# Performance work log

Hardware: AMD Instinct MI355X
Metric: run time of the kernel (lower is better)

## Reference

```python
import jax, jax.numpy as jnp
import numpy as np

NUM_CLS = 80
NUM_CONVS = 4
GROUPS = 32
STRIDES = [8, 16, 32, 64, 128]
SIZES = [32.0, 64.0, 128.0, 256.0, 512.0]
CLS_BIAS_INIT = -float(np.log((1 - 0.01) / 0.01))


def _conv(x, w, b):
    # NCHW 3x3 stride-1 same-pad conv
    y = jax.lax.conv_general_dilated(x, w, (1, 1), 'SAME',
                                     dimension_numbers=('NCHW', 'OIHW', 'NCHW'))
    return y + b[None, :, None, None]


def _group_norm(x, gamma, beta, eps=1e-5):
    B, C, H, W = x.shape
    xr = x.reshape(B, GROUPS, C // GROUPS, H, W)
    m = xr.mean(axis=(2, 3, 4), keepdims=True)
    v = xr.var(axis=(2, 3, 4), keepdims=True)
    xn = ((xr - m) / jnp.sqrt(v + eps)).reshape(B, C, H, W)
    return xn * gamma[None, :, None, None] + beta[None, :, None, None]


def _tower(x, ws, bs, gs, betas):
    # CGR block: Conv -> GroupNorm -> ReLU, repeated NUM_CONVS times
    for i in range(NUM_CONVS):
        x = jax.nn.relu(_group_norm(_conv(x, ws[i], bs[i]), gs[i], betas[i]))
    return x


def _build_anchors(h, w, stride, size):
    half = size / 2.0  # single scale=1, ratio=1 -> one square anchor per cell
    yv, xv = jnp.meshgrid(jnp.arange(h, dtype=jnp.float32),
                          jnp.arange(w, dtype=jnp.float32), indexing='ij')
    grid = jnp.stack([xv, yv, xv, yv], axis=-1)  # [h,w,4]
    delta = jnp.array([-half, -half, half, half], dtype=jnp.float32)
    return ((grid + 0.5) * stride + delta).reshape(-1, 4)  # [h*w,4]


def setup_inputs() -> dict:
    key = jax.random.key(0)
    ks = jax.random.split(key, 16)
    C = 256
    feats = {}
    hw = [80, 40, 20, 10, 5]
    for i, name in enumerate(['p3', 'p4', 'p5', 'p6', 'p7']):
        feats[name] = jax.random.normal(ks[i], (8, C, hw[i], hw[i]), dtype=jnp.float32)
    std = 0.01
    inp = dict(feats)
    # cls tower
    inp['cls_tw'] = jax.random.normal(ks[5], (NUM_CONVS, C, C, 3, 3), jnp.float32) * std
    inp['cls_tb'] = jnp.zeros((NUM_CONVS, C), jnp.float32)
    inp['cls_tg'] = jnp.ones((NUM_CONVS, C), jnp.float32)
    inp['cls_tbeta'] = jnp.zeros((NUM_CONVS, C), jnp.float32)
    # reg tower
    inp['reg_tw'] = jax.random.normal(ks[6], (NUM_CONVS, C, C, 3, 3), jnp.float32) * std
    inp['reg_tb'] = jnp.zeros((NUM_CONVS, C), jnp.float32)
    inp['reg_tg'] = jnp.ones((NUM_CONVS, C), jnp.float32)
    inp['reg_tbeta'] = jnp.zeros((NUM_CONVS, C), jnp.float32)
    # heads (num_anchors = 1)
    inp['cls_hw'] = jax.random.normal(ks[7], (NUM_CLS, C, 3, 3), jnp.float32) * std
    inp['cls_hb'] = jnp.full((NUM_CLS,), CLS_BIAS_INIT, jnp.float32)
    inp['reg_hw'] = jax.random.normal(ks[8], (4, C, 3, 3), jnp.float32) * std
    inp['reg_hb'] = jnp.zeros((4,), jnp.float32)
    inp['iou_hw'] = jax.random.normal(ks[9], (1, C, 3, 3), jnp.float32) * std
    inp['iou_hb'] = jnp.zeros((1,), jnp.float32)
    inp['scales'] = jnp.ones((5,), jnp.float32)
    return inp


def reference(p3, p4, p5, p6, p7,
              cls_tw, cls_tb, cls_tg, cls_tbeta,
              reg_tw, reg_tb, reg_tg, reg_tbeta,
              cls_hw, cls_hb, reg_hw, reg_hb, iou_hw, iou_hb, scales):
    feats = [p3, p4, p5, p6, p7]
    outs = []
    for j, x in enumerate(feats):
        B, _, H, W = x.shape
        ct = _tower(x, cls_tw, cls_tb, cls_tg, cls_tbeta)
        rt = _tower(x, reg_tw, reg_tb, reg_tg, reg_tbeta)
        # heads: permute to NHWC then flatten spatial (num_anchors=1)
        cls = _conv(ct, cls_hw, cls_hb).transpose(0, 2, 3, 1).reshape(B, -1, NUM_CLS)
        reg = _conv(rt, reg_hw, reg_hb).transpose(0, 2, 3, 1).reshape(B, -1, 4) * scales[j]
        iou = _conv(rt, iou_hw, iou_hb).transpose(0, 2, 3, 1).reshape(B, -1, 1)  # on_reg=True
        # decode boxes against anchors
        anchor = _build_anchors(H, W, STRIDES[j], SIZES[j])  # [HW,4]
        awh = anchor[:, 2:] - anchor[:, :2]
        actr = anchor[:, :2] + 0.5 * awh
        xy = reg[..., :2] * awh + actr
        wh = jnp.exp(reg[..., 2:]) * awh
        box = jnp.concatenate([xy - 0.5 * wh, xy + 0.5 * wh], axis=-1)
        outs.append(jnp.concatenate([box, iou, cls], axis=-1))
    return jnp.concatenate(outs, axis=1)  # [B, 8525, 85]
```

## Files before the change

### kernel.cpp

```cpp
#include <hip/hip_runtime.h>
#include <stdint.h>

typedef unsigned short u16;
typedef unsigned int u32;
typedef short short8 __attribute__((ext_vector_type(8)));
typedef float f32x4 __attribute__((ext_vector_type(4)));

struct LevelTab {
  int Hf[5], Wf[5], Hp[5], Wp[5], HW[5], M[5], mtcum[5], aoff[5];
  long xoffp[5], moff[5], ppcum[5], mcum[5];
  float asize[5], astride[5];
};

__device__ __forceinline__ u16 f2bf(float f) {
  u32 u = __float_as_uint(f);
  u = (u + 0x7fffu + ((u >> 16) & 1u)) >> 16;
  return (u16)u;
}
__device__ __forceinline__ float bflo(u32 v) { return __uint_as_float(v << 16); }
__device__ __forceinline__ float bfhi(u32 v) { return __uint_as_float(v & 0xffff0000u); }

__device__ __forceinline__ void gload16(const void* g, void* l) {
  __builtin_amdgcn_global_load_lds((__attribute__((address_space(1))) void*)(g),
                                   (__attribute__((address_space(3))) void*)(l),
                                   16, 0, 0);
}

__global__ __launch_bounds__(256) void prep_tower_w(const float* __restrict__ cls_tw,
                                                    const float* __restrict__ reg_tw,
                                                    u16* __restrict__ W2t) {
  long t = (long)blockIdx.x * 256 + threadIdx.x;
  const long total = 2L * 4 * 256 * 2304;
  if (t >= total) return;
  int ci = (int)(t & 255);
  long u = t >> 8;
  int j = (int)(u % 9); u /= 9;
  int co = (int)(u & 255); u >>= 8;
  int layer = (int)(u & 3);
  int tw = (int)(u >> 2);
  const float* src = tw ? reg_tw : cls_tw;
  float v = src[(((long)layer * 256 + co) * 256 + ci) * 9 + j];
  W2t[t] = f2bf(v);
}

__global__ __launch_bounds__(256) void prep_cls_w(const float* __restrict__ cls_hw,
                                                  u16* __restrict__ W2c) {
  long t = (long)blockIdx.x * 256 + threadIdx.x;
  if (t >= 128L * 2304) return;
  int ci = (int)(t & 255);
  long u = t >> 8;
  int j = (int)(u % 9);
  int co = (int)(u / 9);
  float v = (co < 80) ? cls_hw[(((long)co * 256 + ci) * 9 + j)] : 0.f;
  W2c[t] = f2bf(v);
}

__global__ __launch_bounds__(256) void prep_reg_w(const float* __restrict__ reg_hw,
                                                  const float* __restrict__ iou_hw,
                                                  u16* __restrict__ W2r) {
  long t = (long)blockIdx.x * 256 + threadIdx.x;
  if (t >= 5L * 2304) return;
  int ci = (int)(t & 255);
  long u = t >> 8;
  int j = (int)(u % 9);
  int o = (int)(u / 9);
  float v = (o < 4) ? reg_hw[(((long)o * 256 + ci) * 9 + j)] : iou_hw[(long)ci * 9 + j];
  W2r[t] = f2bf(v);
}

__global__ __launch_bounds__(256) void convert_in(const float* __restrict__ i0, const float* __restrict__ i1,
                                                  const float* __restrict__ i2, const float* __restrict__ i3,
                                                  const float* __restrict__ i4, u16* __restrict__ X0,
                                                  LevelTab lt) {
  long t = (long)blockIdx.x * 256 + threadIdx.x;
  if (t >= lt.ppcum[4] * 32) return;
  const int c8 = (int)(t & 31);
  long pp = t >> 5;
  int lvl = 0;
#pragma unroll
  for (int i = 0; i < 4; ++i) lvl += (pp >= lt.ppcum[i]);
  const long lp = pp - (lvl ? lt.ppcum[lvl - 1] : 0);
  const int Hp = lt.Hp[lvl], Wp = lt.Wp[lvl], Wf = lt.Wf[lvl], HW = lt.HW[lvl];
  const int HpWp = Hp * Wp;
  const int n = (int)(lp / HpWp);
  const int rem = (int)(lp - (long)n * HpWp);
  const int yp = rem / Wp, xp = rem - yp * Wp;
  u16* op = X0 + (lt.xoffp[lvl] + lp) * 256 + c8 * 8;
  if (yp == 0 || yp == Hp - 1 || xp == 0 || xp == Wp - 1) {
    *(uint4*)op = make_uint4(0u, 0u, 0u, 0u);
    return;
  }
  const float* src = lvl == 0 ? i0 : lvl == 1 ? i1 : lvl == 2 ? i2 : lvl == 3 ? i3 : i4;
  const int y = yp - 1, x = xp - 1;
  const long sb = ((long)n * 256 + c8 * 8) * HW + (long)y * Wf + x;
  u32 o4[4];
#pragma unroll
  for (int i = 0; i < 4; ++i) {
    float f0 = src[sb + (long)(2 * i) * HW];
    float f1 = src[sb + (long)(2 * i + 1) * HW];
    o4[i] = (u32)f2bf(f0) | ((u32)f2bf(f1) << 16);
  }
  *(uint4*)op = make_uint4(o4[0], o4[1], o4[2], o4[3]);
}

template <int MODE>
__global__ __launch_bounds__(256, 2) void conv_mfma(
    const u16* __restrict__ XpadA, const u16* __restrict__ XpadB,
    const u16* __restrict__ W2A, const u16* __restrict__ W2B,
    const float* __restrict__ biasA, const float* __restrict__ biasB,
    u16* __restrict__ OtmpA, u16* __restrict__ OtmpB,
    float* __restrict__ Oout, int NP, LevelTab lt) {
  __shared__ __align__(16) u16 sA[3][128 * 32];
  __shared__ __align__(16) u16 sB[3][128 * 32];

  const int nwg = gridDim.x;
  const int qq = nwg >> 3, rr = nwg & 7;
  const int xcd = blockIdx.x & 7, ib = blockIdx.x >> 3;
  const int sid = (xcd < rr ? xcd * (qq + 1) : rr * (qq + 1) + (xcd - rr) * qq) + ib;

  int path, tileId, nt;
  if (MODE == 0) {
    const int tn = (NP == 2) ? (sid >> 1) : sid;
    path = (NP == 2) ? (sid & 1) : 0;
    tileId = tn >> 1;
    nt = tn & 1;
  } else {
    path = 0;
    tileId = sid;
    nt = 0;
  }
  const u16* __restrict__ Xpad = path ? XpadB : XpadA;
  const u16* __restrict__ W2 = path ? W2B : W2A;
  const float* __restrict__ bias = path ? biasB : biasA;
  u16* __restrict__ Otmp = path ? OtmpB : OtmpA;

  int lvl = 0;
#pragma unroll
  for (int i = 0; i < 4; ++i) lvl += (tileId >= lt.mtcum[i]);
  const int mt = tileId - (lvl ? lt.mtcum[lvl - 1] : 0);
  const int Hp = lt.Hp[lvl], Wp = lt.Wp[lvl], Wf = lt.Wf[lvl];
  const int HW = lt.HW[lvl], M = lt.M[lvl];
  const long xbase = lt.xoffp[lvl] * 256;

  const int tid = threadIdx.x;
  const int w = tid >> 6, lane = tid & 63;
  const int rsub = lane >> 2;
  const int r0 = w * 16 + rsub;
  const int q2 = ((lane & 3) - ((lane >> 3) & 3)) & 3;

  long gA[2], gB[2];
#pragma unroll
  for (int i = 0; i < 2; ++i) {
    int ml = mt * 128 + r0 + i * 64;
    if (ml > M - 1) ml = M - 1;
    const int n = ml / HW;
    const int pr = ml - n * HW;
    const int y = pr / Wf;
    const int x = pr - y * Wf;
    gA[i] = xbase + ((long)((n * Hp + y) * Wp + x)) * 256 + q2 * 8;
    gB[i] = (long)(nt * 128 + r0 + i * 64) * 2304 + q2 * 8;
  }

  const int wm = w >> 1, wn = w & 1;
  const int lm = lane & 15;
  const int slot8 = ((((lane >> 4) + ((lane >> 1) & 3)) & 3) << 3);

  f32x4 acc[4][4];
#pragma unroll
  for (int a = 0; a < 4; ++a)
#pragma unroll
    for (int c = 0; c < 4; ++c) acc[a][c] = {0.f, 0.f, 0.f, 0.f};

  auto STAGE = [&](int kk, int buf) {
    const int j = kk >> 3;
    const int c0 = (kk & 7) << 5;
    const int jy = j / 3, jx = j - jy * 3;
    const long aK = ((long)(jy * Wp + jx)) * 256 + c0;
    const long bK = (long)kk << 5;
    gload16(Xpad + gA[0] + aK, sA[buf] + w * 512);
    gload16(Xpad + gA[1] + aK, sA[buf] + 2048 + w * 512);
    gload16(W2 + gB[0] + bK, sB[buf] + w * 512);
    gload16(W2 + gB[1] + bK, sB[buf] + 2048 + w * 512);
  };

  short8 a0[4], b0[4], a1[4], b1[4];
  auto FRAG0 = [&](int cur) {
    const u16* pa = sA[cur];
    const u16* pb = sB[cur];
#pragma unroll
    for (int mi = 0; mi < 4; ++mi)
      a0[mi] = *(const short8*)(pa + ((wm * 64 + mi * 16 + lm) << 5) + slot8);
#pragma unroll
    for (int ni = 0; ni < 4; ++ni)
      b0[ni] = *(const short8*)(pb + ((wn * 64 + ni * 16 + lm) << 5) + slot8);
  };
  auto FRAG1 = [&](int cur) {
    const u16* pa = sA[cur];
    const u16* pb = sB[cur];
#pragma unroll
    for (int mi = 0; mi < 4; ++mi)
      a1[mi] = *(const short8*)(pa + ((wm * 64 + mi * 16 + lm) << 5) + slot8);
#pragma unroll
    for (int ni = 0; ni < 4; ++ni)
      b1[ni] = *(const short8*)(pb + ((wn * 64 + ni * 16 + lm) << 5) + slot8);
  };
  auto MFMA0 = [&]() {
    __builtin_amdgcn_s_setprio(1);
#pragma unroll
    for (int mi = 0; mi < 4; ++mi)
#pragma unroll
      for (int ni = 0; ni < 4; ++ni)
        acc[mi][ni] = __builtin_amdgcn_mfma_f32_16x16x32_bf16(a0[mi], b0[ni], acc[mi][ni], 0, 0, 0);
    __builtin_amdgcn_s_setprio(0);
  };
  auto MFMA1 = [&]() {
    __builtin_amdgcn_s_setprio(1);
#pragma unroll
    for (int mi = 0; mi < 4; ++mi)
#pragma unroll
      for (int ni = 0; ni < 4; ++ni)
        acc[mi][ni] = __builtin_amdgcn_mfma_f32_16x16x32_bf16(a1[mi], b1[ni], acc[mi][ni], 0, 0, 0);
    __builtin_amdgcn_s_setprio(0);
  };

  STAGE(0, 0);
  STAGE(1, 1);
  asm volatile("s_waitcnt vmcnt(4)" ::: "memory");
  __builtin_amdgcn_s_barrier();
  FRAG0(0);
  STAGE(2, 2);

  int rd = 1;
  int st = 0;
  for (int kk = 0; kk < 68; kk += 2) {
    asm volatile("s_waitcnt vmcnt(4)" ::: "memory");
    __builtin_amdgcn_s_barrier();
    FRAG1(rd);
    rd = rd == 2 ? 0 : rd + 1;
    STAGE(kk + 3, st);
    st = st == 2 ? 0 : st + 1;
    MFMA0();
    asm volatile("s_waitcnt vmcnt(4)" ::: "memory");
    __builtin_amdgcn_s_barrier();
    FRAG0(rd);
    rd = rd == 2 ? 0 : rd + 1;
    STAGE(kk + 4, st);
    st = st == 2 ? 0 : st + 1;
    MFMA1();
  }
  asm volatile("s_waitcnt vmcnt(4)" ::: "memory");
  __builtin_amdgcn_s_barrier();
  FRAG1(rd);
  rd = rd == 2 ? 0 : rd + 1;
  STAGE(71, st);
  MFMA0();
  asm volatile("s_waitcnt vmcnt(4)" ::: "memory");
  __builtin_amdgcn_s_barrier();
  FRAG0(rd);
  rd = rd == 2 ? 0 : rd + 1;
  MFMA1();
  asm volatile("s_waitcnt vmcnt(0)" ::: "memory");
  __builtin_amdgcn_s_barrier();
  FRAG1(rd);
  MFMA0();
  MFMA1();

  const int mwb = mt * 128 + wm * 64;
  const int colb = nt * 128 + wn * 64;
  const int rq4 = (lane >> 4) << 2;
#pragma unroll
  for (int ni = 0; ni < 4; ++ni) {
    const int col = colb + ni * 16 + lm;
    if (MODE == 1 && col >= 80) continue;
    const float bv = bias[col];
#pragma unroll
    for (int mi = 0; mi < 4; ++mi) {
      const int rb = mwb + mi * 16 + rq4;
#pragma unroll
      for (int rg = 0; rg < 4; ++rg) {
        const int ml = rb + rg;
        if (ml < M) {
          const float v = acc[mi][ni][rg] + bv;
          if (MODE == 0) {
            Otmp[(lt.moff[lvl] + ml) * 256 + col] = f2bf(v);
          } else {
            const int nb = ml / HW;
            const int pr = ml - nb * HW;
            Oout[((long)nb * 8525 + lt.aoff[lvl] + pr) * 85 + 5 + col] = v;
          }
        }
      }
    }
  }
}

__global__ __launch_bounds__(256) void gn_stats(const u16* __restrict__ tmpA,
                                                const u16* __restrict__ tmpB,
                                                float* __restrict__ stats, LevelTab lt) {
  const int bid = blockIdx.x;
  const int path = bid / 1280;
  const int lb = bid - path * 1280;
  const u16* __restrict__ tmp = path ? tmpB : tmpA;
  const int lvl = lb >> 8, bg = lb & 255, b = bg >> 5, g = bg & 31;
  const int HW = lt.HW[lvl];
  const long base = (lt.moff[lvl] + (long)b * HW) * 256 + g * 8;
  float s = 0.f, ss = 0.f;
  for (int p = threadIdx.x; p < HW; p += 256) {
    const uint4 r = *(const uint4*)(tmp + base + (long)p * 256);
    const u32 u[4] = {r.x, r.y, r.z, r.w};
#pragma unroll
    for (int i = 0; i < 4; ++i) {
      float f0 = bflo(u[i]), f1 = bfhi(u[i]);
      s += f0 + f1;
      ss += f0 * f0 + f1 * f1;
    }
  }
#pragma unroll
  for (int o = 32; o; o >>= 1) {
    s += __shfl_down(s, o);
    ss += __shfl_down(ss, o);
  }
  __shared__ float rs[4], rss[4];
  const int w = threadIdx.x >> 6, lane = threadIdx.x & 63;
  if (lane == 0) { rs[w] = s; rss[w] = ss; }
  __syncthreads();
  if (threadIdx.x == 0) {
    s = rs[0] + rs[1] + rs[2] + rs[3];
    ss = rss[0] + rss[1] + rss[2] + rss[3];
    const float inv = 1.f / (float)(HW * 8);
    const float mean = s * inv;
    const float var = ss * inv - mean * mean;
    stats[bid * 2 + 0] = mean;
    stats[bid * 2 + 1] = rsqrtf(var + 1e-5f);
  }
}

__global__ __launch_bounds__(256) void gn_apply(const u16* __restrict__ tmpA,
                                                const u16* __restrict__ tmpB,
                                                const float* __restrict__ stats,
                                                const float* __restrict__ gammaA,
                                                const float* __restrict__ betaA,
                                                const float* __restrict__ gammaB,
                                                const float* __restrict__ betaB,
                                                u16* __restrict__ poutA, u16* __restrict__ poutB,
                                                int ppBlocks, LevelTab lt) {
  const int path = blockIdx.x / ppBlocks;
  const int xb = blockIdx.x - path * ppBlocks;
  const u16* __restrict__ tmp = path ? tmpB : tmpA;
  const float* __restrict__ gamma = path ? gammaB : gammaA;
  const float* __restrict__ beta = path ? betaB : betaA;
  u16* __restrict__ pout = path ? poutB : poutA;

  long t = (long)xb * 256 + threadIdx.x;
  if (t >= lt.ppcum[4] * 32) return;
  const int c8 = (int)(t & 31);
  long pp = t >> 5;
  int lvl = 0;
#pragma unroll
  for (int i = 0; i < 4; ++i) lvl += (pp >= lt.ppcum[i]);
  const long lp = pp - (lvl ? lt.ppcum[lvl - 1] : 0);
  const int Hp = lt.Hp[lvl], Wp = lt.Wp[lvl], Wf = lt.Wf[lvl], HW = lt.HW[lvl];
  const int HpWp = Hp * Wp;
  const int n = (int)(lp / HpWp);
  const int rem = (int)(lp - (long)n * HpWp);
  const int yp = rem / Wp, xp = rem - yp * Wp;
  u16* op = pout + (lt.xoffp[lvl] + lp) * 256 + c8 * 8;
  if (yp == 0 || yp == Hp - 1 || xp == 0 || xp == Wp - 1) {
    *(uint4*)op = make_uint4(0u, 0u, 0u, 0u);
    return;
  }
  const long m = lt.moff[lvl] + (long)n * HW + (long)(yp - 1) * Wf + (xp - 1);
  const uint4 r = *(const uint4*)(tmp + m * 256 + c8 * 8);
  const int sidx = (path * 1280 + lvl * 256 + n * 32 + c8) * 2;
  const float mean = stats[sidx], rstd = stats[sidx + 1];
  const u32 u[4] = {r.x, r.y, r.z, r.w};
  u32 o4[4];
#pragma unroll
  for (int i = 0; i < 4; ++i) {
    const int c = c8 * 8 + i * 2;
    float f0 = (bflo(u[i]) - mean) * rstd * gamma[c] + beta[c];
    float f1 = (bfhi(u[i]) - mean) * rstd * gamma[c + 1] + beta[c + 1];
    f0 = fmaxf(f0, 0.f);
    f1 = fmaxf(f1, 0.f);
    o4[i] = (u32)f2bf(f0) | ((u32)f2bf(f1) << 16);
  }
  *(uint4*)op = make_uint4(o4[0], o4[1], o4[2], o4[3]);
}

__global__ __launch_bounds__(256) void regiou_decode(const u16* __restrict__ Xp,
                                                     const u16* __restrict__ W2r,
                                                     const float* __restrict__ reg_hb,
                                                     const float* __restrict__ iou_hb,
                                                     const float* __restrict__ scales,
                                                     float* __restrict__ out, LevelTab lt) {
  const long gt = (long)blockIdx.x * 256 + threadIdx.x;
  const int gw = (int)(gt >> 6);
  const int lane = threadIdx.x & 63;
  if (gw >= (int)lt.mcum[4]) return;
  int lvl = 0;
#pragma unroll
  for (int i = 0; i < 4; ++i) lvl += (gw >= (int)lt.mcum[i]);
  const int m = gw - (int)(lvl ? lt.mcum[lvl - 1] : 0);
  const int HW = lt.HW[lvl], Wf = lt.Wf[lvl], Hp = lt.Hp[lvl], Wp = lt.Wp[lvl];
  const int b = m / HW, pr = m - b * HW;
  const int y = pr / Wf, x = pr - y * Wf;
  const long base = (lt.xoffp[lvl] + (long)(b * Hp + y) * Wp + x) * 256 + lane * 4;
  float acc[5] = {0.f, 0.f, 0.f, 0.f, 0.f};
#pragma unroll
  for (int j = 0; j < 9; ++j) {
    const int jy = j / 3, jx = j - jy * 3;
    const uint2 ar = *(const uint2*)(Xp + base + ((long)(jy * Wp + jx)) * 256);
    const float x0 = bflo(ar.x), x1 = bfhi(ar.x), x2 = bflo(ar.y), x3 = bfhi(ar.y);
#pragma unroll
    for (int o = 0; o < 5; ++o) {
      const uint2 wr = *(const uint2*)(W2r + o * 2304 + j * 256 + lane * 4);
      acc[o] += x0 * bflo(wr.x) + x1 * bfhi(wr.x) + x2 * bflo(wr.y) + x3 * bfhi(wr.y);
    }
  }
#pragma unroll
  for (int o = 0; o < 5; ++o)
#pragma unroll
    for (int d = 32; d; d >>= 1) acc[o] += __shfl_down(acc[o], d);
  if (lane == 0) {
    const float sc = scales[lvl];
    const float r0 = (acc[0] + reg_hb[0]) * sc;
    const float r1 = (acc[1] + reg_hb[1]) * sc;
    const float r2 = (acc[2] + reg_hb[2]) * sc;
    const float r3 = (acc[3] + reg_hb[3]) * sc;
    const float iou = acc[4] + iou_hb[0];
    const float st = lt.astride[lvl], sz = lt.asize[lvl];
    const float cx = (x + 0.5f) * st, cy = (y + 0.5f) * st;
    const float xx = r0 * sz + cx, yy = r1 * sz + cy;
    const float ww = expf(r2) * sz, hh = expf(r3) * sz;
    float* o = out + ((long)b * 8525 + lt.aoff[lvl] + pr) * 85;
    o[0] = xx - 0.5f * ww;
    o[1] = yy - 0.5f * hh;
    o[2] = xx + 0.5f * ww;
    o[3] = yy + 0.5f * hh;
    o[4] = iou;
  }
}

extern "C" void kernel_launch(void* const* d_in, const int* in_sizes, int n_in, void* d_out,
                              int out_size, void* d_ws, size_t ws_size, hipStream_t stream) {
  const float* feats[5];
  for (int i = 0; i < 5; ++i) feats[i] = (const float*)d_in[i];
  const float* cls_tw = (const float*)d_in[5];
  const float* cls_tb = (const float*)d_in[6];
  const float* cls_tg = (const float*)d_in[7];
  const float* cls_tbeta = (const float*)d_in[8];
  const float* reg_tw = (const float*)d_in[9];
  const float* reg_tb = (const float*)d_in[10];
  const float* reg_tg = (const float*)d_in[11];
  const float* reg_tbeta = (const float*)d_in[12];
  const float* cls_hw = (const float*)d_in[13];
  const float* cls_hb = (const float*)d_in[14];
  const float* reg_hw = (const float*)d_in[15];
  const float* reg_hb = (const float*)d_in[16];
  const float* iou_hw = (const float*)d_in[17];
  const float* iou_hb = (const float*)d_in[18];
  const float* scales = (const float*)d_in[19];
  float* out = (float*)d_out;

  LevelTab lt;
  const int Hs[5] = {80, 40, 20, 10, 5};
  const float sizes[5] = {32.f, 64.f, 128.f, 256.f, 512.f};
  const float strides[5] = {8.f, 16.f, 32.f, 64.f, 128.f};
  long ppc = 0, mc = 0;
  int mtc = 0, ao = 0;
  for (int i = 0; i < 5; ++i) {
    const int H = Hs[i];
    lt.Hf[i] = H; lt.Wf[i] = H; lt.Hp[i] = H + 2; lt.Wp[i] = H + 2;
    lt.HW[i] = H * H; lt.M[i] = 8 * H * H;
    lt.xoffp[i] = ppc; lt.moff[i] = mc; lt.aoff[i] = ao;
    ppc += 8L * (H + 2) * (H + 2);
    mc += lt.M[i];
    mtc += (lt.M[i] + 127) / 128;
    lt.ppcum[i] = ppc; lt.mcum[i] = mc; lt.mtcum[i] = mtc;
    ao += H * H;
    lt.asize[i] = sizes[i]; lt.astride[i] = strides[i];
  }

  char* ws = (char*)d_ws;
  size_t off = 0;
  auto take = [&](size_t bytes) {
    off = (off + 255) & ~(size_t)255;
    char* p = ws + off;
    off += bytes;
    return p;
  };
  auto alg = [](size_t v) { return (v + 255) & ~(size_t)255; };
  const size_t sizeX = alg((size_t)ppc * 512);
  const size_t sizeT = alg((size_t)mc * 512);
  const size_t wTsz = alg((size_t)2 * 4 * 256 * 2304 * 2);
  const size_t wCsz = alg((size_t)128 * 2304 * 2);
  const size_t wRsz = alg((size_t)5 * 2304 * 2);
  const size_t sSsz = alg((size_t)2 * 1280 * 2 * 4);
  const size_t needMerged = 4 * sizeX + 2 * sizeT + wTsz + wCsz + wRsz + sSsz + 4096;
  const bool MERGED = (ws_size >= needMerged);

  const int ppBlocks = (int)((ppc * 32 + 255) / 256);

  if (MERGED) {
    u16* X0 = (u16*)take(sizeX);
    u16* C1 = (u16*)take(sizeX);
    u16* R0 = (u16*)take(sizeX);
    u16* R1 = (u16*)take(sizeX);
    u16* tmpA = (u16*)take(sizeT);
    u16* tmpB = (u16*)take(sizeT);
    u16* W2t = (u16*)take(wTsz);
    u16* W2c = (u16*)take(wCsz);
    u16* W2r = (u16*)take(wRsz);
    float* stats = (float*)take(sSsz);

    prep_tower_w<<<(int)((2L * 4 * 256 * 2304 + 255) / 256), 256, 0, stream>>>(cls_tw, reg_tw, W2t);
    prep_cls_w<<<(int)((128L * 2304 + 255) / 256), 256, 0, stream>>>(cls_hw, W2c);
    prep_reg_w<<<(int)((5L * 2304 + 255) / 256), 256, 0, stream>>>(reg_hw, iou_hw, W2r);
    convert_in<<<ppBlocks, 256, 0, stream>>>(feats[0], feats[1], feats[2], feats[3], feats[4], X0, lt);

    u16* wrA[4] = {X0, C1, X0, C1};
    u16* wrB[4] = {R0, R1, R0, R1};
    const u16* curA = X0;
    const u16* curB = X0;
    for (int layer = 0; layer < 4; ++layer) {
      const u16* w2A = W2t + (size_t)(0 * 4 + layer) * 256 * 2304;
      const u16* w2B = W2t + (size_t)(1 * 4 + layer) * 256 * 2304;
      conv_mfma<0><<<mtc * 2 * 2, 256, 0, stream>>>(curA, curB, w2A, w2B,
                                                    cls_tb + layer * 256, reg_tb + layer * 256,
                                                    tmpA, tmpB, nullptr, 2, lt);
      gn_stats<<<2 * 1280, 256, 0, stream>>>(tmpA, tmpB, stats, lt);
      gn_apply<<<2 * ppBlocks, 256, 0, stream>>>(tmpA, tmpB, stats,
                                                 cls_tg + layer * 256, cls_tbeta + layer * 256,
                                                 reg_tg + layer * 256, reg_tbeta + layer * 256,
                                                 wrA[layer], wrB[layer], ppBlocks, lt);
      curA = wrA[layer];
      curB = wrB[layer];
    }
    conv_mfma<1><<<mtc, 256, 0, stream>>>(curA, curA, W2c, W2c, cls_hb, cls_hb,
                                          nullptr, nullptr, out, 1, lt);
    regiou_decode<<<(int)((mc * 64 + 255) / 256), 256, 0, stream>>>(curB, W2r, reg_hb, iou_hb,
                                                                    scales, out, lt);
  } else {
    u16* X0 = (u16*)take(sizeX);
    u16* padA = (u16*)take(sizeX);
    u16* padB = (u16*)take(sizeX);
    u16* tmp = (u16*)take(sizeT);
    u16* W2t = (u16*)take(wTsz);
    u16* W2c = (u16*)take(wCsz);
    u16* W2r = (u16*)take(wRsz);
    float* stats = (float*)take(sSsz);

    prep_tower_w<<<(int)((2L * 4 * 256 * 2304 + 255) / 256), 256, 0, stream>>>(cls_tw, reg_tw, W2t);
    prep_cls_w<<<(int)((128L * 2304 + 255) / 256), 256, 0, stream>>>(cls_hw, W2c);
    prep_reg_w<<<(int)((5L * 2304 + 255) / 256), 256, 0, stream>>>(reg_hw, iou_hw, W2r);
    convert_in<<<ppBlocks, 256, 0, stream>>>(feats[0], feats[1], feats[2], feats[3], feats[4], X0, lt);

    u16* pads[2] = {padA, padB};
    for (int tw = 0; tw < 2; ++tw) {
      const float* tb = tw ? reg_tb : cls_tb;
      const float* tg = tw ? reg_tg : cls_tg;
      const float* tbe = tw ? reg_tbeta : cls_tbeta;
      const u16* cur = X0;
      for (int layer = 0; layer < 4; ++layer) {
        const u16* w2 = W2t + (size_t)(tw * 4 + layer) * 256 * 2304;
        conv_mfma<0><<<mtc * 2, 256, 0, stream>>>(cur, cur, w2, w2, tb + layer * 256,
                                                  tb + layer * 256, tmp, tmp, nullptr, 1, lt);
        gn_stats<<<1280, 256, 0, stream>>>(tmp, tmp, stats, lt);
        u16* nxt = pads[layer & 1];
        gn_apply<<<ppBlocks, 256, 0, stream>>>(tmp, tmp, stats, tg + layer * 256,
                                               tbe + layer * 256, tg + layer * 256,
                                               tbe + layer * 256, nxt, nxt, ppBlocks, lt);
        cur = nxt;
      }
      if (tw == 0) {
        conv_mfma<1><<<mtc, 256, 0, stream>>>(cur, cur, W2c, W2c, cls_hb, cls_hb,
                                              nullptr, nullptr, out, 1, lt);
      } else {
        regiou_decode<<<(int)((mc * 64 + 255) / 256), 256, 0, stream>>>(cur, W2r, reg_hb, iou_hb,
                                                                        scales, out, lt);
      }
    }
  }
}
```

Baseline: 1.522 ms.

## Fuse GroupNorm stats and apply into one kernel, pre-zero pad borders

Merges the separate GroupNorm statistics and normalize+ReLU kernels into a single kernel per (batch, group, level). Each block computes mean and rstd, then rereads its slice and writes the normalized padded output. This removes one launch and the stats round-trip per layer. Border zeroing moves into convert_in, which zeroes the pad rings of all ping-pong buffers once so the fused kernel only writes interiors. The conv tile-to-path mapping also changes from interleaved to split halves. The fused kernel uses only 2560 blocks with a serial per-thread loop over HW, which may cut parallelism for large levels compared with the former per-pixel apply kernel.

```diff
diff --git a/kernel.cpp b/kernel.cpp
--- a/kernel.cpp
+++ b/kernel.cpp
@@ -71,7 +71,8 @@
 __global__ __launch_bounds__(256) void convert_in(const float* __restrict__ i0, const float* __restrict__ i1,
                                                   const float* __restrict__ i2, const float* __restrict__ i3,
                                                   const float* __restrict__ i4, u16* __restrict__ X0,
-                                                  LevelTab lt) {
+                                                  u16* __restrict__ Z1, u16* __restrict__ Z2,
+                                                  u16* __restrict__ Z3, LevelTab lt) {
   long t = (long)blockIdx.x * 256 + threadIdx.x;
   if (t >= lt.ppcum[4] * 32) return;
   const int c8 = (int)(t & 31);
@@ -85,9 +86,13 @@
   const int n = (int)(lp / HpWp);
   const int rem = (int)(lp - (long)n * HpWp);
   const int yp = rem / Wp, xp = rem - yp * Wp;
-  u16* op = X0 + (lt.xoffp[lvl] + lp) * 256 + c8 * 8;
+  const long oof = (lt.xoffp[lvl] + lp) * 256 + c8 * 8;
   if (yp == 0 || yp == Hp - 1 || xp == 0 || xp == Wp - 1) {
-    *(uint4*)op = make_uint4(0u, 0u, 0u, 0u);
+    const uint4 z = make_uint4(0u, 0u, 0u, 0u);
+    *(uint4*)(X0 + oof) = z;
+    *(uint4*)(Z1 + oof) = z;
+    *(uint4*)(Z2 + oof) = z;
+    *(uint4*)(Z3 + oof) = z;
     return;
   }
   const float* src = lvl == 0 ? i0 : lvl == 1 ? i1 : lvl == 2 ? i2 : lvl == 3 ? i3 : i4;
@@ -100,7 +105,7 @@
     float f1 = src[sb + (long)(2 * i + 1) * HW];
     o4[i] = (u32)f2bf(f0) | ((u32)f2bf(f1) << 16);
   }
-  *(uint4*)op = make_uint4(o4[0], o4[1], o4[2], o4[3]);
+  *(uint4*)(X0 + oof) = make_uint4(o4[0], o4[1], o4[2], o4[3]);
 }
 
 template <int MODE>
@@ -120,10 +125,17 @@
 
   int path, tileId, nt;
   if (MODE == 0) {
-    const int tn = (NP == 2) ? (sid >> 1) : sid;
-    path = (NP == 2) ? (sid & 1) : 0;
-    tileId = tn >> 1;
-    nt = tn & 1;
+    if (NP == 2) {
+      const int half = nwg >> 1;
+      path = (sid >= half) ? 1 : 0;
+      const int inner = sid - path * half;
+      tileId = inner >> 1;
+      nt = inner & 1;
+    } else {
+      path = 0;
+      tileId = sid >> 1;
+      nt = sid & 1;
+    }
   } else {
     path = 0;
     tileId = sid;
@@ -294,16 +306,25 @@
   }
 }
 
-__global__ __launch_bounds__(256) void gn_stats(const u16* __restrict__ tmpA,
+__global__ __launch_bounds__(256) void gn_fused(const u16* __restrict__ tmpA,
                                                 const u16* __restrict__ tmpB,
-                                                float* __restrict__ stats, LevelTab lt) {
+                                                const float* __restrict__ gammaA,
+                                                const float* __restrict__ betaA,
+                                                const float* __restrict__ gammaB,
+                                                const float* __restrict__ betaB,
+                                                u16* __restrict__ poutA, u16* __restrict__ poutB,
+                                                LevelTab lt) {
   const int bid = blockIdx.x;
   const int path = bid / 1280;
   const int lb = bid - path * 1280;
   const u16* __restrict__ tmp = path ? tmpB : tmpA;
+  const float* __restrict__ gamma = path ? gammaB : gammaA;
+  const float* __restrict__ beta = path ? betaB : betaA;
+  u16* __restrict__ pout = path ? poutB : poutA;
   const int lvl = lb >> 8, bg = lb & 255, b = bg >> 5, g = bg & 31;
   const int HW = lt.HW[lvl];
   const long base = (lt.moff[lvl] + (long)b * HW) * 256 + g * 8;
+
   float s = 0.f, ss = 0.f;
   for (int p = threadIdx.x; p < HW; p += 256) {
     const uint4 r = *(const uint4*)(tmp + base + (long)p * 256);
@@ -321,6 +342,7 @@
     ss += __shfl_down(ss, o);
   }
   __shared__ float rs[4], rss[4];
+  __shared__ float smean, srstd;
   const int w = threadIdx.x >> 6, lane = threadIdx.x & 63;
   if (lane == 0) { rs[w] = s; rss[w] = ss; }
   __syncthreads();
@@ -330,61 +352,36 @@
     const float inv = 1.f / (float)(HW * 8);
     const float mean = s * inv;
     const float var = ss * inv - mean * mean;
-    stats[bid * 2 + 0] = mean;
-    stats[bid * 2 + 1] = rsqrtf(var + 1e-5f);
-  }
-}
-
-__global__ __launch_bounds__(256) void gn_apply(const u16* __restrict__ tmpA,
-                                                const u16* __restrict__ tmpB,
-                                                const float* __restrict__ stats,
-                                                const float* __restrict__ gammaA,
-                                                const float* __restrict__ betaA,
-                                                const float* __restrict__ gammaB,
-                                                const float* __restrict__ betaB,
-                                                u16* __restrict__ poutA, u16* __restrict__ poutB,
-                                                int ppBlocks, LevelTab lt) {
-  const int path = blockIdx.x / ppBlocks;
-  const int xb = blockIdx.x - path * ppBlocks;
-  const u16* __restrict__ tmp = path ? tmpB : tmpA;
-  const float* __restrict__ gamma = path ? gammaB : gammaA;
-  const float* __restrict__ beta = path ? betaB : betaA;
-  u16* __restrict__ pout = path ? poutB : poutA;
-
-  long t = (long)xb * 256 + threadIdx.x;
-  if (t >= lt.ppcum[4] * 32) return;
-  const int c8 = (int)(t & 31);
-  long pp = t >> 5;
-  int lvl = 0;
-#pragma unroll
-  for (int i = 0; i < 4; ++i) lvl += (pp >= lt.ppcum[i]);
-  const long lp = pp - (lvl ? lt.ppcum[lvl - 1] : 0);
-  const int Hp = lt.Hp[lvl], Wp = lt.Wp[lvl], Wf = lt.Wf[lvl], HW = lt.HW[lvl];
-  const int HpWp = Hp * Wp;
-  const int n = (int)(lp / HpWp);
-  const int rem = (int)(lp - (long)n * HpWp);
-  const int yp = rem / Wp, xp = rem - yp * Wp;
-  u16* op = pout + (lt.xoffp[lvl] + lp) * 256 + c8 * 8;
-  if (yp == 0 || yp == Hp - 1 || xp == 0 || xp == Wp - 1) {
-    *(uint4*)op = make_uint4(0u, 0u, 0u, 0u);
-    return;
-  }
-  const long m = lt.moff[lvl] + (long)n * HW + (long)(yp - 1) * Wf + (xp - 1);
-  const uint4 r = *(const uint4*)(tmp + m * 256 + c8 * 8);
-  const int sidx = (path * 1280 + lvl * 256 + n * 32 + c8) * 2;
-  const float mean = stats[sidx], rstd = stats[sidx + 1];
-  const u32 u[4] = {r.x, r.y, r.z, r.w};
-  u32 o4[4];
-#pragma unroll
-  for (int i = 0; i < 4; ++i) {
-    const int c = c8 * 8 + i * 2;
-    float f0 = (bflo(u[i]) - mean) * rstd * gamma[c] + beta[c];
-    float f1 = (bfhi(u[i]) - mean) * rstd * gamma[c + 1] + beta[c + 1];
-    f0 = fmaxf(f0, 0.f);
-    f1 = fmaxf(f1, 0.f);
-    o4[i] = (u32)f2bf(f0) | ((u32)f2bf(f1) << 16);
-  }
-  *(uint4*)op = make_uint4(o4[0], o4[1], o4[2], o4[3]);
+    smean = mean;
+    srstd = rsqrtf(var + 1e-5f);
+  }
+  __syncthreads();
+  const float mean = smean, rstd = srstd;
+
+  float gm[8], bt[8];
+#pragma unroll
+  for (int i = 0; i < 8; ++i) {
+    gm[i] = gamma[g * 8 + i];
+    bt[i] = beta[g * 8 + i];
+  }
+  const int Wf = lt.Wf[lvl], Wp = lt.Wp[lvl];
+  const int HpWp = lt.Hp[lvl] * Wp;
+  u16* pb = pout + (lt.xoffp[lvl] + (long)b * HpWp) * 256 + g * 8;
+  for (int p = threadIdx.x; p < HW; p += 256) {
+    const uint4 r = *(const uint4*)(tmp + base + (long)p * 256);
+    const int y = p / Wf, x = p - y * Wf;
+    const u32 u[4] = {r.x, r.y, r.z, r.w};
+    u32 o4[4];
+#pragma unroll
+    for (int i = 0; i < 4; ++i) {
+      float f0 = (bflo(u[i]) - mean) * rstd * gm[2 * i] + bt[2 * i];
+      float f1 = (bfhi(u[i]) - mean) * rstd * gm[2 * i + 1] + bt[2 * i + 1];
+      f0 = fmaxf(f0, 0.f);
+      f1 = fmaxf(f1, 0.f);
+      o4[i] = (u32)f2bf(f0) | ((u32)f2bf(f1) << 16);
+    }
+    *(uint4*)(pb + ((long)(y + 1) * Wp + (x + 1)) * 256) = make_uint4(o4[0], o4[1], o4[2], o4[3]);
+  }
 }
 
 __global__ __launch_bounds__(256) void regiou_decode(const u16* __restrict__ Xp,
@@ -495,8 +492,7 @@
   const size_t wTsz = alg((size_t)2 * 4 * 256 * 2304 * 2);
   const size_t wCsz = alg((size_t)128 * 2304 * 2);
   const size_t wRsz = alg((size_t)5 * 2304 * 2);
-  const size_t sSsz = alg((size_t)2 * 1280 * 2 * 4);
-  const size_t needMerged = 4 * sizeX + 2 * sizeT + wTsz + wCsz + wRsz + sSsz + 4096;
+  const size_t needMerged = 4 * sizeX + 2 * sizeT + wTsz + wCsz + wRsz + 4096;
   const bool MERGED = (ws_size >= needMerged);
 
   const int ppBlocks = (int)((ppc * 32 + 255) / 256);
@@ -511,12 +507,12 @@
     u16* W2t = (u16*)take(wTsz);
     u16* W2c = (u16*)take(wCsz);
     u16* W2r = (u16*)take(wRsz);
-    float* stats = (float*)take(sSsz);
 
     prep_tower_w<<<(int)((2L * 4 * 256 * 2304 + 255) / 256), 256, 0, stream>>>(cls_tw, reg_tw, W2t);
     prep_cls_w<<<(int)((128L * 2304 + 255) / 256), 256, 0, stream>>>(cls_hw, W2c);
     prep_reg_w<<<(int)((5L * 2304 + 255) / 256), 256, 0, stream>>>(reg_hw, iou_hw, W2r);
-    convert_in<<<ppBlocks, 256, 0, stream>>>(feats[0], feats[1], feats[2], feats[3], feats[4], X0, lt);
+    convert_in<<<ppBlocks, 256, 0, stream>>>(feats[0], feats[1], feats[2], feats[3], feats[4],
+                                             X0, C1, R0, R1, lt);
 
     u16* wrA[4] = {X0, C1, X0, C1};
     u16* wrB[4] = {R0, R1, R0, R1};
@@ -528,11 +524,10 @@
       conv_mfma<0><<<mtc * 2 * 2, 256, 0, stream>>>(curA, curB, w2A, w2B,
                                                     cls_tb + layer * 256, reg_tb + layer * 256,
                                                     tmpA, tmpB, nullptr, 2, lt);
-      gn_stats<<<2 * 1280, 256, 0, stream>>>(tmpA, tmpB, stats, lt);
-      gn_apply<<<2 * ppBlocks, 256, 0, stream>>>(tmpA, tmpB, stats,
-                                                 cls_tg + layer * 256, cls_tbeta + layer * 256,
-                                                 reg_tg + layer * 256, reg_tbeta + layer * 256,
-                                                 wrA[layer], wrB[layer], ppBlocks, lt);
+      gn_fused<<<2 * 1280, 256, 0, stream>>>(tmpA, tmpB,
+                                             cls_tg + layer * 256, cls_tbeta + layer * 256,
+                                             reg_tg + layer * 256, reg_tbeta + layer * 256,
+                                             wrA[layer], wrB[layer], lt);
       curA = wrA[layer];
       curB = wrB[layer];
     }
@@ -548,12 +543,12 @@
     u16* W2t = (u16*)take(wTsz);
     u16* W2c = (u16*)take(wCsz);
     u16* W2r = (u16*)take(wRsz);
-    float* stats = (float*)take(sSsz);
 
     prep_tower_w<<<(int)((2L * 4 * 256 * 2304 + 255) / 256), 256, 0, stream>>>(cls_tw, reg_tw, W2t);
     prep_cls_w<<<(int)((128L * 2304 + 255) / 256), 256, 0, stream>>>(cls_hw, W2c);
     prep_reg_w<<<(int)((5L * 2304 + 255) / 256), 256, 0, stream>>>(reg_hw, iou_hw, W2r);
-    convert_in<<<ppBlocks, 256, 0, stream>>>(feats[0], feats[1], feats[2], feats[3], feats[4], X0, lt);
+    convert_in<<<ppBlocks, 256, 0, stream>>>(feats[0], feats[1], feats[2], feats[3], feats[4],
+                                             X0, padA, padB, padA, lt);
 
     u16* pads[2] = {padA, padB};
     for (int tw = 0; tw < 2; ++tw) {
@@ -565,11 +560,9 @@
         const u16* w2 = W2t + (size_t)(tw * 4 + layer) * 256 * 2304;
         conv_mfma<0><<<mtc * 2, 256, 0, stream>>>(cur, cur, w2, w2, tb + layer * 256,
                                                   tb + layer * 256, tmp, tmp, nullptr, 1, lt);
-        gn_stats<<<1280, 256, 0, stream>>>(tmp, tmp, stats, lt);
         u16* nxt = pads[layer & 1];
-        gn_apply<<<ppBlocks, 256, 0, stream>>>(tmp, tmp, stats, tg + layer * 256,
-                                               tbe + layer * 256, tg + layer * 256,
-                                               tbe + layer * 256, nxt, nxt, ppBlocks, lt);
+        gn_fused<<<1280, 256, 0, stream>>>(tmp, tmp, tg + layer * 256, tbe + layer * 256,
+                                           tg + layer * 256, tbe + layer * 256, nxt, nxt, lt);
         cur = nxt;
       }
       if (tw == 0) {
```

Result: slower. 1.911 ms (+25.6%).

## Split GroupNorm stats into chunked coalesced partial sums plus a finalize kernel

Applied to the files above, without the earlier changes.

The per-(batch,group) GN stats kernel, which read 16-byte strided slices with one block per group, is replaced by gn_part. In gn_part each block covers all 32 groups of one (level, batch, spatial chunk of 800 pixels), so a 256-thread block reads full 512-byte rows coalesced and writes partial sums. A small gn_final kernel reduces the chunks into mean and rstd. The conv tile mapping also changes so that the two tower paths occupy contiguous halves of the grid instead of interleaving. The cost is one extra kernel launch per layer and a partial-sum buffer.

```diff
diff --git a/kernel.cpp b/kernel.cpp
--- a/kernel.cpp
+++ b/kernel.cpp
@@ -6,8 +6,12 @@
 typedef short short8 __attribute__((ext_vector_type(8)));
 typedef float f32x4 __attribute__((ext_vector_type(4)));
 
+#define GN_CHUNK 800
+#define GN_MAXCH 8
+
 struct LevelTab {
   int Hf[5], Wf[5], Hp[5], Wp[5], HW[5], M[5], mtcum[5], aoff[5];
+  int gch[5];
   long xoffp[5], moff[5], ppcum[5], mcum[5];
   float asize[5], astride[5];
 };
@@ -120,10 +124,17 @@
 
   int path, tileId, nt;
   if (MODE == 0) {
-    const int tn = (NP == 2) ? (sid >> 1) : sid;
-    path = (NP == 2) ? (sid & 1) : 0;
-    tileId = tn >> 1;
-    nt = tn & 1;
+    if (NP == 2) {
+      const int half = nwg >> 1;
+      path = (sid >= half) ? 1 : 0;
+      const int inner = sid - path * half;
+      tileId = inner >> 1;
+      nt = inner & 1;
+    } else {
+      path = 0;
+      tileId = sid >> 1;
+      nt = sid & 1;
+    }
   } else {
     path = 0;
     tileId = sid;
@@ -294,20 +305,33 @@
   }
 }
 
-__global__ __launch_bounds__(256) void gn_stats(const u16* __restrict__ tmpA,
-                                                const u16* __restrict__ tmpB,
-                                                float* __restrict__ stats, LevelTab lt) {
+__global__ __launch_bounds__(256) void gn_part(const u16* __restrict__ tmpA,
+                                               const u16* __restrict__ tmpB,
+                                               float* __restrict__ part, int perPath,
+                                               LevelTab lt) {
   const int bid = blockIdx.x;
-  const int path = bid / 1280;
-  const int lb = bid - path * 1280;
+  const int path = bid / perPath;
+  int r = bid - path * perPath;
+  int lvl = 0;
+#pragma unroll
+  for (int i = 0; i < 4; ++i) {
+    const int c = 8 * lt.gch[i];
+    if (r >= c) { r -= c; lvl = i + 1; } else break;
+  }
+  const int b = r / lt.gch[lvl];
+  const int chunk = r - b * lt.gch[lvl];
   const u16* __restrict__ tmp = path ? tmpB : tmpA;
-  const int lvl = lb >> 8, bg = lb & 255, b = bg >> 5, g = bg & 31;
   const int HW = lt.HW[lvl];
-  const long base = (lt.moff[lvl] + (long)b * HW) * 256 + g * 8;
+  const int start = chunk * GN_CHUNK;
+  const int end = (start + GN_CHUNK < HW) ? start + GN_CHUNK : HW;
+
+  const int tid = threadIdx.x;
+  const int c8 = tid & 31, po = tid >> 5;
+  const long base = (lt.moff[lvl] + (long)b * HW) * 256 + c8 * 8;
   float s = 0.f, ss = 0.f;
-  for (int p = threadIdx.x; p < HW; p += 256) {
-    const uint4 r = *(const uint4*)(tmp + base + (long)p * 256);
-    const u32 u[4] = {r.x, r.y, r.z, r.w};
+  for (int p = start + po; p < end; p += 8) {
+    const uint4 r4 = *(const uint4*)(tmp + base + (long)p * 256);
+    const u32 u[4] = {r4.x, r4.y, r4.z, r4.w};
 #pragma unroll
     for (int i = 0; i < 4; ++i) {
       float f0 = bflo(u[i]), f1 = bfhi(u[i]);
@@ -315,24 +339,39 @@
       ss += f0 * f0 + f1 * f1;
     }
   }
-#pragma unroll
-  for (int o = 32; o; o >>= 1) {
-    s += __shfl_down(s, o);
-    ss += __shfl_down(ss, o);
-  }
-  __shared__ float rs[4], rss[4];
-  const int w = threadIdx.x >> 6, lane = threadIdx.x & 63;
-  if (lane == 0) { rs[w] = s; rss[w] = ss; }
+  s += __shfl_down(s, 32);
+  ss += __shfl_down(ss, 32);
+  __shared__ float rs[4][32], rss[4][32];
+  const int w = tid >> 6, lane = tid & 63;
+  if (lane < 32) { rs[w][lane] = s; rss[w][lane] = ss; }
   __syncthreads();
-  if (threadIdx.x == 0) {
-    s = rs[0] + rs[1] + rs[2] + rs[3];
-    ss = rss[0] + rss[1] + rss[2] + rss[3];
-    const float inv = 1.f / (float)(HW * 8);
-    const float mean = s * inv;
-    const float var = ss * inv - mean * mean;
-    stats[bid * 2 + 0] = mean;
-    stats[bid * 2 + 1] = rsqrtf(var + 1e-5f);
-  }
+  if (tid < 32) {
+    const float S = rs[0][tid] + rs[1][tid] + rs[2][tid] + rs[3][tid];
+    const float SS = rss[0][tid] + rss[1][tid] + rss[2][tid] + rss[3][tid];
+    const long slot = ((long)((path * 1280 + lvl * 256 + b * 32 + tid) * GN_MAXCH + chunk)) * 2;
+    part[slot] = S;
+    part[slot + 1] = SS;
+  }
+}
+
+__global__ __launch_bounds__(256) void gn_final(const float* __restrict__ part,
+                                                float* __restrict__ stats, LevelTab lt) {
+  const int idx = blockIdx.x * 256 + threadIdx.x;
+  if (idx >= 2 * 1280) return;
+  const int lb = idx % 1280;
+  const int lvl = lb >> 8;
+  const int nch = lt.gch[lvl];
+  float s = 0.f, ss = 0.f;
+  const long sbase = (long)idx * GN_MAXCH * 2;
+  for (int c = 0; c < nch; ++c) {
+    s += part[sbase + c * 2];
+    ss += part[sbase + c * 2 + 1];
+  }
+  const float inv = 1.f / (float)(lt.HW[lvl] * 8);
+  const float mean = s * inv;
+  const float var = ss * inv - mean * mean;
+  stats[idx * 2 + 0] = mean;
+  stats[idx * 2 + 1] = rsqrtf(var + 1e-5f);
 }
 
 __global__ __launch_bounds__(256) void gn_apply(const u16* __restrict__ tmpA,
@@ -467,19 +506,22 @@
   const float sizes[5] = {32.f, 64.f, 128.f, 256.f, 512.f};
   const float strides[5] = {8.f, 16.f, 32.f, 64.f, 128.f};
   long ppc = 0, mc = 0;
-  int mtc = 0, ao = 0;
+  int mtc = 0, ao = 0, chTot = 0;
   for (int i = 0; i < 5; ++i) {
     const int H = Hs[i];
     lt.Hf[i] = H; lt.Wf[i] = H; lt.Hp[i] = H + 2; lt.Wp[i] = H + 2;
     lt.HW[i] = H * H; lt.M[i] = 8 * H * H;
+    lt.gch[i] = (H * H + GN_CHUNK - 1) / GN_CHUNK;
     lt.xoffp[i] = ppc; lt.moff[i] = mc; lt.aoff[i] = ao;
     ppc += 8L * (H + 2) * (H + 2);
     mc += lt.M[i];
     mtc += (lt.M[i] + 127) / 128;
     lt.ppcum[i] = ppc; lt.mcum[i] = mc; lt.mtcum[i] = mtc;
     ao += H * H;
+    chTot += lt.gch[i];
     lt.asize[i] = sizes[i]; lt.astride[i] = strides[i];
   }
+  const int perPath = 8 * chTot;
 
   char* ws = (char*)d_ws;
   size_t off = 0;
@@ -495,8 +537,9 @@
   const size_t wTsz = alg((size_t)2 * 4 * 256 * 2304 * 2);
   const size_t wCsz = alg((size_t)128 * 2304 * 2);
   const size_t wRsz = alg((size_t)5 * 2304 * 2);
-  const size_t sSsz = alg((size_t)2 * 1280 * 2 * 4);
-  const size_t needMerged = 4 * sizeX + 2 * sizeT + wTsz + wCsz + wRsz + sSsz + 4096;
+  const size_t pSz = alg((size_t)2 * 1280 * GN_MAXCH * 2 * 4);
+  const size_t sSz = alg((size_t)2 * 1280 * 2 * 4);
+  const size_t needMerged = 4 * sizeX + 2 * sizeT + wTsz + wCsz + wRsz + pSz + sSz + 4096;
   const bool MERGED = (ws_size >= needMerged);
 
   const int ppBlocks = (int)((ppc * 32 + 255) / 256);
@@ -511,12 +554,14 @@
     u16* W2t = (u16*)take(wTsz);
     u16* W2c = (u16*)take(wCsz);
     u16* W2r = (u16*)take(wRsz);
-    float* stats = (float*)take(sSsz);
+    float* part = (float*)take(pSz);
+    float* stats = (float*)take(sSz);
 
     prep_tower_w<<<(int)((2L * 4 * 256 * 2304 + 255) / 256), 256, 0, stream>>>(cls_tw, reg_tw, W2t);
     prep_cls_w<<<(int)((128L * 2304 + 255) / 256), 256, 0, stream>>>(cls_hw, W2c);
     prep_reg_w<<<(int)((5L * 2304 + 255) / 256), 256, 0, stream>>>(reg_hw, iou_hw, W2r);
-    convert_in<<<ppBlocks, 256, 0, stream>>>(feats[0], feats[1], feats[2], feats[3], feats[4], X0, lt);
+    convert_in<<<ppBlocks, 256, 0, stream>>>(feats[0], feats[1], feats[2], feats[3], feats[4],
+                                             X0, lt);
 
     u16* wrA[4] = {X0, C1, X0, C1};
     u16* wrB[4] = {R0, R1, R0, R1};
@@ -528,7 +573,8 @@
       conv_mfma<0><<<mtc * 2 * 2, 256, 0, stream>>>(curA, curB, w2A, w2B,
                                                     cls_tb + layer * 256, reg_tb + layer * 256,
                                                     tmpA, tmpB, nullptr, 2, lt);
-      gn_stats<<<2 * 1280, 256, 0, stream>>>(tmpA, tmpB, stats, lt);
+      gn_part<<<2 * perPath, 256, 0, stream>>>(tmpA, tmpB, part, perPath, lt);
+      gn_final<<<10, 256, 0, stream>>>(part, stats, lt);
       gn_apply<<<2 * ppBlocks, 256, 0, stream>>>(tmpA, tmpB, stats,
                                                  cls_tg + layer * 256, cls_tbeta + layer * 256,
                                                  reg_tg + layer * 256, reg_tbeta + layer * 256,
@@ -548,12 +594,14 @@
     u16* W2t = (u16*)take(wTsz);
     u16* W2c = (u16*)take(wCsz);
     u16* W2r = (u16*)take(wRsz);
-    float* stats = (float*)take(sSsz);
+    float* part = (float*)take(pSz);
+    float* stats = (float*)take(sSz);
 
     prep_tower_w<<<(int)((2L * 4 * 256 * 2304 + 255) / 256), 256, 0, stream>>>(cls_tw, reg_tw, W2t);
     prep_cls_w<<<(int)((128L * 2304 + 255) / 256), 256, 0, stream>>>(cls_hw, W2c);
     prep_reg_w<<<(int)((5L * 2304 + 255) / 256), 256, 0, stream>>>(reg_hw, iou_hw, W2r);
-    convert_in<<<ppBlocks, 256, 0, stream>>>(feats[0], feats[1], feats[2], feats[3], feats[4], X0, lt);
+    convert_in<<<ppBlocks, 256, 0, stream>>>(feats[0], feats[1], feats[2], feats[3], feats[4],
+                                             X0, lt);
 
     u16* pads[2] = {padA, padB};
     for (int tw = 0; tw < 2; ++tw) {
@@ -565,7 +613,8 @@
         const u16* w2 = W2t + (size_t)(tw * 4 + layer) * 256 * 2304;
         conv_mfma<0><<<mtc * 2, 256, 0, stream>>>(cur, cur, w2, w2, tb + layer * 256,
                                                   tb + layer * 256, tmp, tmp, nullptr, 1, lt);
-        gn_stats<<<1280, 256, 0, stream>>>(tmp, tmp, stats, lt);
+        gn_part<<<perPath, 256, 0, stream>>>(tmp, tmp, part, perPath, lt);
+        gn_final<<<10, 256, 0, stream>>>(part, stats, lt);
         u16* nxt = pads[layer & 1];
         gn_apply<<<ppBlocks, 256, 0, stream>>>(tmp, tmp, stats, tg + layer * 256,
                                                tbe + layer * 256, tg + layer * 256,
```

After: 1.346 ms, median of 2. -11.6%, faster.
